# Optimization experiments

Measured on AMD Instinct MI355X. Metric: run time of the kernel, lower is better.

Reference implementation:

```python
import jax, jax.numpy as jnp
import numpy as np

N_NODES = 100000
N_EDGES = 640000
IN_CH = 128
HID = 128


def setup_inputs() -> dict:
    key = jax.random.key(0)
    k1, k2, k3, k4, k5 = jax.random.split(key, 5)
    z = jax.random.normal(k1, (N_NODES, IN_CH), dtype=jnp.float32)
    edge_index = jax.random.randint(k2, (2, N_EDGES), 0, N_NODES, dtype=jnp.int64)
    # Linear layers: stored as [in, out] for x @ W + b
    s1 = 1.0 / np.sqrt(2 * IN_CH)
    W1 = jax.random.uniform(k3, (2 * IN_CH, HID), minval=-s1, maxval=s1, dtype=jnp.float32)
    b1 = jnp.zeros((HID,), dtype=jnp.float32)
    s2 = 1.0 / np.sqrt(HID)
    W2 = jax.random.uniform(k4, (HID, 1), minval=-s2, maxval=s2, dtype=jnp.float32)
    b2 = jnp.zeros((1,), dtype=jnp.float32)
    return {"z": z, "edge_index": edge_index, "W1": W1, "b1": b1, "W2": W2, "b2": b2}


def reference(z, edge_index, W1, b1, W2, b2):
    # gather source/destination node embeddings and concat -> [E, 2*C]
    h = jnp.concatenate([z[edge_index[0]], z[edge_index[1]]], axis=-1)
    h = jax.nn.relu(h @ W1 + b1)  # [E, HID]; Dropout(0.2) is identity in eval
    out = h @ W2 + b2             # [E, 1]
    return out.squeeze(-1)        # [E]
```

## Files before the change

### kernel.cpp

```cpp
#include <hip/hip_runtime.h>
#include <hip/hip_bf16.h>

typedef short bf16x8 __attribute__((ext_vector_type(8)));
typedef float f32x4  __attribute__((ext_vector_type(4)));
typedef unsigned short u16;

static __device__ __forceinline__ u16 f2bf(float f) {
    unsigned u = __float_as_uint(f);
    u += 0x7FFFu + ((u >> 16) & 1u);
    return (u16)(u >> 16);
}
static __device__ __forceinline__ float bf2f(u16 b) {
    return __uint_as_float(((unsigned)b) << 16);
}

__global__ void prep_w(const float* __restrict__ W1, u16* __restrict__ Wl) {
    int idx = blockIdx.x * 256 + threadIdx.x;
    if (idx >= 256 * 128) return;
    int r = idx >> 7;
    int q = idx & 127;
    int k = (r < 128) ? r : (r - 128);
    int c = (r < 128) ? q : (q + 128);
    Wl[c * 128 + k] = f2bf(W1[idx]);
}

#define BM 128
__global__ __launch_bounds__(256, 1) void node_gemm(
    const float* __restrict__ z,
    const u16*   __restrict__ Wl,
    u16*         __restrict__ PQ,
    int M)
{
    __shared__ char As[BM * 256];
    const int tid  = threadIdx.x;
    const int lane = tid & 63;
    const int wave = tid >> 6;
    const int m0   = blockIdx.x * BM;

    #pragma unroll
    for (int i = 0; i < (BM * 32) / 256; ++i) {
        int ci  = tid + i * 256;
        int row = ci >> 5;
        int c4  = ci & 31;
        float4 v = make_float4(0.f, 0.f, 0.f, 0.f);
        if (m0 + row < M)
            v = *(const float4*)(z + (size_t)(m0 + row) * 128 + c4 * 4);
        ushort4 b;
        b.x = f2bf(v.x); b.y = f2bf(v.y); b.z = f2bf(v.z); b.w = f2bf(v.w);
        int byte = row * 256 + ((c4 * 8) ^ ((row & 7) << 4));
        *(ushort4*)(As + byte) = b;
    }
    __syncthreads();

    f32x4 acc[8][4];
    #pragma unroll
    for (int mi = 0; mi < 8; ++mi)
        #pragma unroll
        for (int nf = 0; nf < 4; ++nf)
            acc[mi][nf] = (f32x4){0.f, 0.f, 0.f, 0.f};

    const int g  = lane >> 4;
    const int ln = lane & 15;
    const int n0 = wave * 64;

    #pragma unroll
    for (int ks = 0; ks < 4; ++ks) {
        bf16x8 b[4];
        #pragma unroll
        for (int nf = 0; nf < 4; ++nf) {
            int c = n0 + nf * 16 + ln;
            b[nf] = *(const bf16x8*)(Wl + c * 128 + ks * 32 + g * 8);
        }
        #pragma unroll
        for (int mi = 0; mi < 8; ++mi) {
            int row  = mi * 16 + ln;
            int byte = row * 256 + ((ks * 64 + g * 16) ^ ((row & 7) << 4));
            bf16x8 a = *(const bf16x8*)(As + byte);
            #pragma unroll
            for (int nf = 0; nf < 4; ++nf)
                acc[mi][nf] = __builtin_amdgcn_mfma_f32_16x16x32_bf16(
                    a, b[nf], acc[mi][nf], 0, 0, 0);
        }
    }

    #pragma unroll
    for (int mi = 0; mi < 8; ++mi) {
        #pragma unroll
        for (int nf = 0; nf < 4; ++nf) {
            #pragma unroll
            for (int r = 0; r < 4; ++r) {
                int row = m0 + mi * 16 + g * 4 + r;
                if (row < M) {
                    int col = n0 + nf * 16 + ln;
                    PQ[(size_t)row * 256 + col] = f2bf(acc[mi][nf][r]);
                }
            }
        }
    }
}

__global__ __launch_bounds__(256) void edge_mlp(
    const int* __restrict__ ei,
    const u16* __restrict__ PQ,
    const float* __restrict__ b1,
    const float* __restrict__ W2,
    const float* __restrict__ b2,
    float* __restrict__ out,
    int E)
{
    int gid = blockIdx.x * 256 + threadIdx.x;
    int e   = gid >> 4;
    if (e >= E) return;
    int sub = gid & 15;

    int s = ei[e];
    int d = ei[E + e];

    uint4 pv = *(const uint4*)(PQ + (size_t)s * 256 + sub * 8);
    uint4 qv = *(const uint4*)(PQ + (size_t)d * 256 + 128 + sub * 8);
    float4 b1a = *(const float4*)(b1 + sub * 8);
    float4 b1b = *(const float4*)(b1 + sub * 8 + 4);
    float4 w2a = *(const float4*)(W2 + sub * 8);
    float4 w2b = *(const float4*)(W2 + sub * 8 + 4);

    const u16* pu = (const u16*)&pv;
    const u16* qu = (const u16*)&qv;
    float bb[8] = {b1a.x, b1a.y, b1a.z, b1a.w, b1b.x, b1b.y, b1b.z, b1b.w};
    float ww[8] = {w2a.x, w2a.y, w2a.z, w2a.w, w2b.x, w2b.y, w2b.z, w2b.w};

    float acc = 0.f;
    #pragma unroll
    for (int j = 0; j < 8; ++j) {
        float h = bf2f(pu[j]) + bf2f(qu[j]) + bb[j];
        h = fmaxf(h, 0.f);
        acc = fmaf(h, ww[j], acc);
    }
    acc += __shfl_xor(acc, 1);
    acc += __shfl_xor(acc, 2);
    acc += __shfl_xor(acc, 4);
    acc += __shfl_xor(acc, 8);

    if (sub == 0) out[e] = acc + b2[0];
}

extern "C" void kernel_launch(void* const* d_in, const int* in_sizes, int n_in,
                              void* d_out, int out_size, void* d_ws, size_t ws_size,
                              hipStream_t stream) {
    const float* z  = (const float*)d_in[0];
    const int*   ei = (const int*)d_in[1];
    const float* W1 = (const float*)d_in[2];
    const float* b1 = (const float*)d_in[3];
    const float* W2 = (const float*)d_in[4];
    const float* b2 = (const float*)d_in[5];
    float* out = (float*)d_out;

    const int M = in_sizes[0] / 128;
    const int E = in_sizes[1] / 2;

    u16* Wl = (u16*)d_ws;
    u16* PQ = (u16*)((char*)d_ws + 65536);

    hipLaunchKernelGGL(prep_w, dim3(128), dim3(256), 0, stream, W1, Wl);

    int gb = (M + BM - 1) / BM;
    hipLaunchKernelGGL(node_gemm, dim3(gb), dim3(256), 0, stream, z, Wl, PQ, M);

    int eb = (E * 16 + 255) / 256;
    hipLaunchKernelGGL(edge_mlp, dim3(eb), dim3(256), 0, stream,
                       ei, PQ, b1, W2, b2, out, E);
}
```

Before: 87.37 us.

## Transpose MFMA operands for packed PQ stores and process two edges per thread group

The node GEMM swaps the A/B operands of the MFMA so each lane holds four consecutive output columns of one node, which lets the PQ writes be packed 8-byte stores instead of scattered 2-byte stores. Launch bounds are raised to allow two blocks per CU. The edge kernel now handles two edges per 16-lane group, using vector loads of the indices and a float2 output store, with twice as many gathers in flight per thread. This adds register pressure and a tail-handling branch.

```diff
diff --git a/kernel.cpp b/kernel.cpp
--- a/kernel.cpp
+++ b/kernel.cpp
@@ -13,6 +13,9 @@
 static __device__ __forceinline__ float bf2f(u16 b) {
     return __uint_as_float(((unsigned)b) << 16);
 }
+static __device__ __forceinline__ unsigned pack2(float lo, float hi) {
+    return (unsigned)f2bf(lo) | ((unsigned)f2bf(hi) << 16);
+}
 
 __global__ void prep_w(const float* __restrict__ W1, u16* __restrict__ Wl) {
     int idx = blockIdx.x * 256 + threadIdx.x;
@@ -25,7 +28,7 @@
 }
 
 #define BM 128
-__global__ __launch_bounds__(256, 1) void node_gemm(
+__global__ __launch_bounds__(256, 2) void node_gemm(
     const float* __restrict__ z,
     const u16*   __restrict__ Wl,
     u16*         __restrict__ PQ,
@@ -54,46 +57,43 @@
 
     f32x4 acc[8][4];
     #pragma unroll
-    for (int mi = 0; mi < 8; ++mi)
+    for (int mf = 0; mf < 8; ++mf)
         #pragma unroll
-        for (int nf = 0; nf < 4; ++nf)
-            acc[mi][nf] = (f32x4){0.f, 0.f, 0.f, 0.f};
+        for (int ci = 0; ci < 4; ++ci)
+            acc[mf][ci] = (f32x4){0.f, 0.f, 0.f, 0.f};
 
     const int g  = lane >> 4;
     const int ln = lane & 15;
-    const int n0 = wave * 64;
+    const int c0 = wave * 64;
 
     #pragma unroll
     for (int ks = 0; ks < 4; ++ks) {
-        bf16x8 b[4];
+        bf16x8 a[4];
         #pragma unroll
-        for (int nf = 0; nf < 4; ++nf) {
-            int c = n0 + nf * 16 + ln;
-            b[nf] = *(const bf16x8*)(Wl + c * 128 + ks * 32 + g * 8);
-        }
+        for (int ci = 0; ci < 4; ++ci)
+            a[ci] = *(const bf16x8*)(Wl + (c0 + ci * 16 + ln) * 128 + ks * 32 + g * 8);
         #pragma unroll
-        for (int mi = 0; mi < 8; ++mi) {
-            int row  = mi * 16 + ln;
+        for (int mf = 0; mf < 8; ++mf) {
+            int row  = mf * 16 + ln;
             int byte = row * 256 + ((ks * 64 + g * 16) ^ ((row & 7) << 4));
-            bf16x8 a = *(const bf16x8*)(As + byte);
+            bf16x8 b = *(const bf16x8*)(As + byte);
             #pragma unroll
-            for (int nf = 0; nf < 4; ++nf)
-                acc[mi][nf] = __builtin_amdgcn_mfma_f32_16x16x32_bf16(
-                    a, b[nf], acc[mi][nf], 0, 0, 0);
+            for (int ci = 0; ci < 4; ++ci)
+                acc[mf][ci] = __builtin_amdgcn_mfma_f32_16x16x32_bf16(
+                    a[ci], b, acc[mf][ci], 0, 0, 0);
         }
     }
 
     #pragma unroll
-    for (int mi = 0; mi < 8; ++mi) {
-        #pragma unroll
-        for (int nf = 0; nf < 4; ++nf) {
+    for (int mf = 0; mf < 8; ++mf) {
+        int node = m0 + mf * 16 + ln;
+        if (node < M) {
             #pragma unroll
-            for (int r = 0; r < 4; ++r) {
-                int row = m0 + mi * 16 + g * 4 + r;
-                if (row < M) {
-                    int col = n0 + nf * 16 + ln;
-                    PQ[(size_t)row * 256 + col] = f2bf(acc[mi][nf][r]);
-                }
+            for (int ci = 0; ci < 4; ++ci) {
+                uint2 w;
+                w.x = pack2(acc[mf][ci][0], acc[mf][ci][1]);
+                w.y = pack2(acc[mf][ci][2], acc[mf][ci][3]);
+                *(uint2*)(PQ + (size_t)node * 256 + c0 + ci * 16 + g * 4) = w;
             }
         }
     }
@@ -108,39 +108,61 @@
     float* __restrict__ out,
     int E)
 {
-    int gid = blockIdx.x * 256 + threadIdx.x;
-    int e   = gid >> 4;
-    if (e >= E) return;
-    int sub = gid & 15;
+    int gid  = blockIdx.x * 256 + threadIdx.x;
+    int e0   = (gid >> 4) * 2;
+    int sub  = gid & 15;
+    if (e0 >= E) return;
+    bool two = (e0 + 1) < E;
 
-    int s = ei[e];
-    int d = ei[E + e];
+    int2 ss, dd;
+    if (two) {
+        ss = *(const int2*)(ei + e0);
+        dd = *(const int2*)(ei + E + e0);
+    } else {
+        ss.x = ei[e0];     ss.y = ss.x;
+        dd.x = ei[E + e0]; dd.y = dd.x;
+    }
 
-    uint4 pv = *(const uint4*)(PQ + (size_t)s * 256 + sub * 8);
-    uint4 qv = *(const uint4*)(PQ + (size_t)d * 256 + 128 + sub * 8);
+    uint4 p0 = *(const uint4*)(PQ + (size_t)ss.x * 256 + sub * 8);
+    uint4 q0 = *(const uint4*)(PQ + (size_t)dd.x * 256 + 128 + sub * 8);
+    uint4 p1 = *(const uint4*)(PQ + (size_t)ss.y * 256 + sub * 8);
+    uint4 q1 = *(const uint4*)(PQ + (size_t)dd.y * 256 + 128 + sub * 8);
+
     float4 b1a = *(const float4*)(b1 + sub * 8);
     float4 b1b = *(const float4*)(b1 + sub * 8 + 4);
     float4 w2a = *(const float4*)(W2 + sub * 8);
     float4 w2b = *(const float4*)(W2 + sub * 8 + 4);
-
-    const u16* pu = (const u16*)&pv;
-    const u16* qu = (const u16*)&qv;
     float bb[8] = {b1a.x, b1a.y, b1a.z, b1a.w, b1b.x, b1b.y, b1b.z, b1b.w};
     float ww[8] = {w2a.x, w2a.y, w2a.z, w2a.w, w2b.x, w2b.y, w2b.z, w2b.w};
 
-    float acc = 0.f;
+    const u16* p0u = (const u16*)&p0;
+    const u16* q0u = (const u16*)&q0;
+    const u16* p1u = (const u16*)&p1;
+    const u16* q1u = (const u16*)&q1;
+
+    float acc0 = 0.f, acc1 = 0.f;
     #pragma unroll
     for (int j = 0; j < 8; ++j) {
-        float h = bf2f(pu[j]) + bf2f(qu[j]) + bb[j];
-        h = fmaxf(h, 0.f);
-        acc = fmaf(h, ww[j], acc);
+        float h0 = bf2f(p0u[j]) + bf2f(q0u[j]) + bb[j];
+        float h1 = bf2f(p1u[j]) + bf2f(q1u[j]) + bb[j];
+        acc0 = fmaf(fmaxf(h0, 0.f), ww[j], acc0);
+        acc1 = fmaf(fmaxf(h1, 0.f), ww[j], acc1);
     }
-    acc += __shfl_xor(acc, 1);
-    acc += __shfl_xor(acc, 2);
-    acc += __shfl_xor(acc, 4);
-    acc += __shfl_xor(acc, 8);
+    #pragma unroll
+    for (int m = 1; m < 16; m <<= 1) {
+        acc0 += __shfl_xor(acc0, m);
+        acc1 += __shfl_xor(acc1, m);
+    }
 
-    if (sub == 0) out[e] = acc + b2[0];
+    if (sub == 0) {
+        float bias = b2[0];
+        if (two) {
+            float2 o = make_float2(acc0 + bias, acc1 + bias);
+            *(float2*)(out + e0) = o;
+        } else {
+            out[e0] = acc0 + bias;
+        }
+    }
 }
 
 extern "C" void kernel_launch(void* const* d_in, const int* in_sizes, int n_in,
@@ -165,7 +187,7 @@
     int gb = (M + BM - 1) / BM;
     hipLaunchKernelGGL(node_gemm, dim3(gb), dim3(256), 0, stream, z, Wl, PQ, M);
 
-    int eb = (E * 16 + 255) / 256;
+    int eb = (E * 8 + 255) / 256;
     hipLaunchKernelGGL(edge_mlp, dim3(eb), dim3(256), 0, stream,
                        ei, PQ, b1, W2, b2, out, E);
 }
```

Measured after the change: 88.40 us. About the same (+1.2%).
